# Kernel tuning notes

Measured on AMD Instinct MI355X. Metric: run time of the kernel, lower is better.

## Reference

```python
import jax, jax.numpy as jnp
from jax import lax
import numpy as np

VOCAB = 50257
EMB = 768
HID = [1024, 1024, 1024]
B, S = 2, 2048
LN_EPS_RNN = 1e-5   # torch default inside MinGRU layers
LN_EPS_OUT = 0.0    # NLPModel passes bias=False into LayerNorm's eps slot


def _layernorm(x, w, b, eps):
    mu = jnp.mean(x, axis=-1, keepdims=True)
    var = jnp.var(x, axis=-1, keepdims=True)
    return (x - mu) * lax.rsqrt(var + eps) * w + b


def _log_g(x):
    # log of g(x) = where(x>=0, x+0.5, sigmoid(x)), computed stably in log space
    return jnp.where(x >= 0, jnp.log(jax.nn.relu(x) + 0.5), -jax.nn.softplus(-x))


def _mingru_scan(gate, hidden, h0):
    # gate, hidden: [B,S,H]; h0: [B,1,H] (positive). Log-space parallel scan.
    log_coeffs = -jax.nn.softplus(gate)              # log(1-z)
    log_values = -jax.nn.softplus(-gate) + _log_g(hidden)  # log(z) + log g(h~)
    log_coeffs = jnp.pad(log_coeffs, ((0, 0), (1, 0), (0, 0)))
    log_values = jnp.concatenate([jnp.log(h0), log_values], axis=1)
    a_star = jnp.cumsum(log_coeffs, axis=1)
    log_h = a_star + lax.cumlogsumexp(log_values - a_star, axis=1)
    return jnp.exp(log_h)[:, 1:]                     # [B,S,H]


def setup_inputs() -> dict:
    key = jax.random.key(0)
    ks = jax.random.split(key, 8)
    inp = {}
    inp["ids"] = jax.random.randint(ks[0], (B, S), 0, VOCAB)
    inp["emb_W"] = jax.random.normal(ks[1], (VOCAB, EMB)) * 0.02
    dims = [EMB] + HID
    for l, (i, o) in enumerate(zip(dims[:-1], dims[1:])):
        inp[f"ln{l}_w"] = jnp.ones((i,))
        inp[f"ln{l}_b"] = jnp.zeros((i,))
        inp[f"gates{l}_W"] = jax.random.normal(jax.random.fold_in(key, 10 + l), (2 * o, i)) * (1.0 / np.sqrt(i))
    inp["res0_W"] = jax.random.normal(ks[2], (HID[0], EMB)) * (1.0 / np.sqrt(EMB))
    inp["lnf_w"] = jnp.ones((HID[-1],))
    inp["lnf_b"] = jnp.zeros((HID[-1],))
    inp["fc_W"] = jax.random.normal(ks[3], (VOCAB, HID[-1])) * 0.02
    inp["fc_b"] = jnp.zeros((VOCAB,))
    return inp


def reference(ids, emb_W, ln0_w, ln0_b, gates0_W, res0_W,
              ln1_w, ln1_b, gates1_W, ln2_w, ln2_b, gates2_W,
              lnf_w, lnf_b, fc_W, fc_b):
    x = emb_W[ids]                                   # [B,S,EMB]
    layers = [
        (ln0_w, ln0_b, gates0_W, res0_W),
        (ln1_w, ln1_b, gates1_W, None),
        (ln2_w, ln2_b, gates2_W, None),
    ]
    inp = x
    for ln_w, ln_b, gW, resW in layers:
        out_dim = gW.shape[0] // 2
        xn = _layernorm(inp, ln_w, ln_b, LN_EPS_RNN)
        gh = jnp.einsum('bsi,oi->bso', xn, gW)       # bias=False for minGRU
        gate, hidden = jnp.split(gh, 2, axis=-1)
        h0 = jnp.full((inp.shape[0], 1, out_dim), 0.5, dtype=inp.dtype)  # g(0)=0.5
        out = _mingru_scan(gate, hidden, h0)
        res = inp if resW is None else jnp.einsum('bsi,oi->bso', inp, resW)
        inp = out + res                              # residual, dropout=0
    x = _layernorm(inp, lnf_w, lnf_b, LN_EPS_OUT)
    logits = jnp.einsum('bsh,vh->bsv', x, fc_W) + fc_b
    return logits
```

## Files before the change

kernel.cpp:

```cpp
#include <hip/hip_runtime.h>
#include <stdint.h>
#include <stddef.h>


typedef __attribute__((ext_vector_type(4))) float f32x4;
typedef __attribute__((ext_vector_type(8))) short bf16x8;
typedef __attribute__((ext_vector_type(4))) unsigned short u16x4;
typedef float f32x4u __attribute__((vector_size(16), aligned(4)));

__device__ __forceinline__ unsigned short f2bf(float f) {
  unsigned int u = __float_as_uint(f);
  u += 0x7FFFu + ((u >> 16) & 1u);
  return (unsigned short)(u >> 16);
}
__device__ __forceinline__ float bf2f(unsigned short u) {
  return __uint_as_float(((unsigned int)u) << 16);
}

__device__ __forceinline__ void gload16(const void* g, void* l) {
  __builtin_amdgcn_global_load_lds(
      (const __attribute__((address_space(1))) void*)g,
      (__attribute__((address_space(3))) void*)l, 16, 0, 0);
}

#define MEMFENCE asm volatile("" ::: "memory")

__global__ __launch_bounds__(256) void cvt_kernel(
    const float* __restrict__ in, unsigned short* __restrict__ out, int n8) {
  int i = blockIdx.x * 256 + threadIdx.x;
  int stride = gridDim.x * 256;
  for (; i < n8; i += stride) {
    const float4* p = (const float4*)in + (size_t)i * 2;
    float4 a = p[0], b = p[1];
    bf16x8 o;
    o[0] = (short)f2bf(a.x); o[1] = (short)f2bf(a.y);
    o[2] = (short)f2bf(a.z); o[3] = (short)f2bf(a.w);
    o[4] = (short)f2bf(b.x); o[5] = (short)f2bf(b.y);
    o[6] = (short)f2bf(b.z); o[7] = (short)f2bf(b.w);
    *(bf16x8*)(out + (size_t)i * 8) = o;
  }
}

__global__ __launch_bounds__(256) void embed_kernel(
    const int* __restrict__ ids, const float* __restrict__ embW,
    unsigned short* __restrict__ xbf) {
  int tok = blockIdx.x;
  int id = ids[tok];
  const float* src = embW + (size_t)id * 768;
  unsigned short* dst = xbf + (size_t)tok * 768;
  for (int j = threadIdx.x; j < 768; j += 256) dst[j] = f2bf(src[j]);
}

template <int BF16IN, int D>
__global__ __launch_bounds__(256) void ln_kernel(
    const void* __restrict__ xin, const float* __restrict__ w,
    const float* __restrict__ b, unsigned short* __restrict__ xout,
    float eps) {
  constexpr int NV = D / 256;
  int row = blockIdx.x;
  int tid = threadIdx.x;
  int lane = tid & 63, wid = tid >> 6;
  const float* xf = (const float*)xin;
  const unsigned short* xb = (const unsigned short*)xin;
  float vals[NV];
  float s = 0.f, ss = 0.f;
#pragma unroll
  for (int i = 0; i < NV; i++) {
    size_t idx = (size_t)row * D + i * 256 + tid;
    float v = BF16IN ? bf2f(xb[idx]) : xf[idx];
    vals[i] = v;
    s += v;
    ss += v * v;
  }
  for (int off = 32; off; off >>= 1) {
    s += __shfl_down(s, off);
    ss += __shfl_down(ss, off);
  }
  __shared__ float red[8];
  if (lane == 0) { red[wid] = s; red[4 + wid] = ss; }
  __syncthreads();
  s = red[0] + red[1] + red[2] + red[3];
  ss = red[4] + red[5] + red[6] + red[7];
  constexpr float invD = 1.f / (float)D;
  float mu = s * invD;
  float var = ss * invD - mu * mu;
  float inv = rsqrtf(var + eps);
#pragma unroll
  for (int i = 0; i < NV; i++) {
    int col = i * 256 + tid;
    size_t idx = (size_t)row * D + col;
    float y = (vals[i] - mu) * inv * w[col] + b[col];
    xout[idx] = f2bf(y);
  }
}

template <int BF16OUT>
__global__ __launch_bounds__(256) void gemm_bt(
    const unsigned short* __restrict__ A, const unsigned short* __restrict__ B,
    void* __restrict__ Cout, int M, int N, int K) {
  __shared__ __align__(16) char smem[16896];
  unsigned short* lsA = (unsigned short*)smem;
  unsigned short* lsB = (unsigned short*)(smem + 8192);
  float* lsC = (float*)smem;

  const int tid = threadIdx.x;
  const int lane = tid & 63;
  const int wid = __builtin_amdgcn_readfirstlane(tid >> 6);
  const int row0 = blockIdx.y * 128;
  const int col0 = blockIdx.x * 128;

  const int srow = tid >> 2;
  const int skg = (tid & 3) * 8;

  const unsigned short* gA0 = A + (size_t)(row0 + srow) * K + skg;
  const unsigned short* gA1 = A + (size_t)(row0 + 64 + srow) * K + skg;
  const unsigned short* gB0 = B + (size_t)(col0 + srow) * K + skg;
  const unsigned short* gB1 = B + (size_t)(col0 + 64 + srow) * K + skg;

  char* ldsA0 = (char*)lsA + wid * 1024;
  char* ldsA1 = (char*)lsA + 4096 + wid * 1024;
  char* ldsB0 = (char*)lsB + wid * 1024;
  char* ldsB1 = (char*)lsB + 4096 + wid * 1024;

  const int wm = wid >> 1, wn = wid & 1;
  const unsigned short* pA = lsA + (wm * 64 + (lane & 15)) * 32 + (lane >> 4) * 8;
  const unsigned short* pB = lsB + (wn * 64 + (lane & 15)) * 32 + (lane >> 4) * 8;

  f32x4 acc[4][4] = {};

  for (int k0 = 0; k0 < K; k0 += 32) {
    gload16(gA0 + k0, ldsA0);
    gload16(gA1 + k0, ldsA1);
    gload16(gB0 + k0, ldsB0);
    gload16(gB1 + k0, ldsB1);
    __syncthreads();
    bf16x8 af[4], bfr[4];
#pragma unroll
    for (int i = 0; i < 4; i++) af[i] = *(const bf16x8*)(pA + i * 512);
#pragma unroll
    for (int i = 0; i < 4; i++) bfr[i] = *(const bf16x8*)(pB + i * 512);
#pragma unroll
    for (int i = 0; i < 4; i++)
#pragma unroll
      for (int j = 0; j < 4; j++)
        acc[i][j] = __builtin_amdgcn_mfma_f32_16x16x32_bf16(bfr[j], af[i],
                                                            acc[i][j], 0, 0, 0);
    __syncthreads();
  }

  const int mloc = lane & 15;
  const int ng = (lane >> 4) * 4;
  const int LDC = 132;
  const int trow = tid >> 5;
  const int tcol = (tid & 31) * 4;
#pragma unroll
  for (int c = 0; c < 4; c++) {
    if (wm == (c >> 1)) {
      const int i0 = 2 * (c & 1);
#pragma unroll
      for (int ii = 0; ii < 2; ii++)
#pragma unroll
        for (int j = 0; j < 4; j++)
          *(f32x4*)(lsC + (ii * 16 + mloc) * LDC + wn * 64 + j * 16 + ng) =
              acc[i0 + ii][j];
    }
    __syncthreads();
#pragma unroll
    for (int rr = 0; rr < 4; rr++) {
      const int r = rr * 8 + trow;
      const size_t gr = row0 + c * 32 + r;
      f32x4 v = *(const f32x4*)(lsC + r * LDC + tcol);
      if (!BF16OUT) {
        *(f32x4*)((float*)Cout + gr * N + col0 + tcol) = v;
      } else {
        u16x4 o;
#pragma unroll
        for (int q = 0; q < 4; q++) o[q] = f2bf(v[q]);
        *(u16x4*)((unsigned short*)Cout + gr * N + col0 + tcol) = o;
      }
    }
    __syncthreads();
  }
}

__global__ __launch_bounds__(512) void gemm_final256(
    const unsigned short* __restrict__ A, const unsigned short* __restrict__ B,
    float* __restrict__ C, const float* __restrict__ bias, int M, int N,
    int K) {
  __shared__ __align__(16) char smem[131072];
  float* const lsC = (float*)smem;

  const int t = threadIdx.x;
  const int l = t & 63;
  const int w = __builtin_amdgcn_readfirstlane(t >> 6);
  const int wm = w >> 2, wn = w & 3;
  const int row0 = blockIdx.x * 256;
  const int col0 = blockIdx.y * 256;

  const int srow = t >> 3;
  const int sg = ((t & 7) ^ (srow & 7)) * 8;
  const unsigned short* aS0 = A + (size_t)(row0 + srow) * K + sg;
  const unsigned short* aS1 = A + (size_t)(row0 + 64 + srow) * K + sg;
  const unsigned short* aS2 = A + (size_t)(row0 + 128 + srow) * K + sg;
  const unsigned short* aS3 = A + (size_t)(row0 + 192 + srow) * K + sg;
  int b0 = min(col0 + srow, N - 1);
  int b1 = min(col0 + 64 + srow, N - 1);
  int b2 = min(col0 + 128 + srow, N - 1);
  int b3 = min(col0 + 192 + srow, N - 1);
  const unsigned short* bS0 = B + (size_t)b0 * K + sg;
  const unsigned short* bS1 = B + (size_t)b1 * K + sg;
  const unsigned short* bS2 = B + (size_t)b2 * K + sg;
  const unsigned short* bS3 = B + (size_t)b3 * K + sg;
  const int wOff = w * 1024;

  const int aRowB = (wm * 128 + (l & 15)) * 128;
  const int bRowB = (wn * 64 + (l & 15)) * 128;
  const int gk0 = ((l >> 4) ^ (l & 7)) * 16;
  const int gk1 = ((4 + (l >> 4)) ^ (l & 7)) * 16;

  f32x4 acc[8][4] = {};

#define STAGE(BUF, KOFF)                       \
  do {                                         \
    char* a_ = smem + (BUF) * 65536;           \
    char* b_ = a_ + 32768;                     \
    gload16(aS0 + (KOFF), a_ + wOff);          \
    gload16(aS1 + (KOFF), a_ + 8192 + wOff);   \
    gload16(aS2 + (KOFF), a_ + 16384 + wOff);  \
    gload16(aS3 + (KOFF), a_ + 24576 + wOff);  \
    gload16(bS0 + (KOFF), b_ + wOff);          \
    gload16(bS1 + (KOFF), b_ + 8192 + wOff);   \
    gload16(bS2 + (KOFF), b_ + 16384 + wOff);  \
    gload16(bS3 + (KOFF), b_ + 24576 + wOff);  \
  } while (0)

  STAGE(0, 0);

  const int NK = K >> 6;
  for (int kt = 0; kt < NK; ++kt) {
    const int cur = kt & 1;
    const char* aB = smem + cur * 65536;
    const char* bB = aB + 32768;

    if (kt + 1 < NK) {
      STAGE(cur ^ 1, (kt + 1) << 6);
      asm volatile("s_waitcnt vmcnt(8)" ::: "memory");
    } else {
      asm volatile("s_waitcnt vmcnt(0)" ::: "memory");
    }
    __builtin_amdgcn_s_barrier();
    MEMFENCE;

    bf16x8 bf[4][2];
#pragma unroll
    for (int j = 0; j < 4; j++) {
      bf[j][0] = *(const bf16x8*)(bB + bRowB + j * 2048 + gk0);
      bf[j][1] = *(const bf16x8*)(bB + bRowB + j * 2048 + gk1);
    }
#pragma unroll
    for (int h = 0; h < 2; h++) {
      bf16x8 af[4][2];
#pragma unroll
      for (int i = 0; i < 4; i++) {
        af[i][0] = *(const bf16x8*)(aB + aRowB + (h * 4 + i) * 2048 + gk0);
        af[i][1] = *(const bf16x8*)(aB + aRowB + (h * 4 + i) * 2048 + gk1);
      }
#pragma unroll
      for (int i = 0; i < 4; i++)
#pragma unroll
        for (int j = 0; j < 4; j++) {
          acc[h * 4 + i][j] = __builtin_amdgcn_mfma_f32_16x16x32_bf16(
              bf[j][0], af[i][0], acc[h * 4 + i][j], 0, 0, 0);
          acc[h * 4 + i][j] = __builtin_amdgcn_mfma_f32_16x16x32_bf16(
              bf[j][1], af[i][1], acc[h * 4 + i][j], 0, 0, 0);
        }
    }

    MEMFENCE;
    __builtin_amdgcn_s_barrier();
    MEMFENCE;
  }
#undef STAGE

  const int mloc = l & 15;
  const int ng = (l >> 4) * 4;
  const int LDC = 260;
#pragma unroll
  for (int c = 0; c < 8; c++) {
    if (wm == (c >> 2)) {
      const int fr0 = (c & 3) * 2;
#pragma unroll
      for (int ii = 0; ii < 2; ii++)
#pragma unroll
        for (int j = 0; j < 4; j++)
          *(f32x4*)(lsC + (ii * 16 + mloc) * LDC + wn * 64 + j * 16 + ng) =
              acc[fr0 + ii][j];
    }
    __syncthreads();
#pragma unroll
    for (int rr = 0; rr < 4; rr++) {
      const int r = rr * 8 + (t >> 6);
      const size_t gr = row0 + c * 32 + r;
      f32x4 v = *(const f32x4*)(lsC + r * LDC + (t & 63) * 4);
      const int n0 = col0 + (t & 63) * 4;
      if (col0 + 256 <= N) {
        const f32x4u bv = *(const f32x4u*)(bias + n0);
        f32x4u o;
#pragma unroll
        for (int q = 0; q < 4; q++) o[q] = v[q] + bv[q];
        __builtin_nontemporal_store(o, (f32x4u*)(C + gr * N + n0));
      } else {
#pragma unroll
        for (int q = 0; q < 4; q++)
          if (n0 + q < N) C[gr * N + n0 + q] = v[q] + bias[n0 + q];
      }
    }
    __syncthreads();
  }
}

__device__ __forceinline__ void gru_step(float gate, float hid, float& a,
                                         float& g) {
  a = 1.f / (1.f + expf(gate));
  g = (hid >= 0.f) ? (hid + 0.5f) : 1.f / (1.f + expf(-hid));
}

__global__ __launch_bounds__(256) void scan_compose(
    const unsigned short* __restrict__ gh, float* __restrict__ Acl,
    float* __restrict__ Vcl) {
  int ck = blockIdx.x;
  int hp = blockIdx.y * 256 + threadIdx.x;
  int b = hp >> 10, h = hp & 1023;
  const unsigned short* gb = gh + ((size_t)(b * 2048 + ck * 64)) * 2048 + h;
  float A = 1.f, V = 0.f;
  for (int t = 0; t < 64; t++) {
    float gate = bf2f(gb[(size_t)t * 2048]);
    float hid = bf2f(gb[(size_t)t * 2048 + 1024]);
    float a, g;
    gru_step(gate, hid, a, g);
    V = a * V + (1.f - a) * g;
    A *= a;
  }
  size_t i = (size_t)(b * 32 + ck) * 1024 + h;
  Acl[i] = A;
  Vcl[i] = V;
}

__global__ __launch_bounds__(256) void scan_prefix(
    const float* __restrict__ Acl, const float* __restrict__ Vcl,
    float* __restrict__ Hin) {
  int hp = blockIdx.x * 256 + threadIdx.x;
  int b = hp >> 10, h = hp & 1023;
  float hr = 0.5f;
  for (int ck = 0; ck < 32; ck++) {
    size_t i = (size_t)(b * 32 + ck) * 1024 + h;
    Hin[i] = hr;
    hr = Acl[i] * hr + Vcl[i];
  }
}

template <int RESBF>
__global__ __launch_bounds__(256) void scan_emit(
    const unsigned short* __restrict__ gh, const float* __restrict__ Hin,
    const void* __restrict__ res, float* __restrict__ xout) {
  int ck = blockIdx.x;
  int hp = blockIdx.y * 256 + threadIdx.x;
  int b = hp >> 10, h = hp & 1023;
  const unsigned short* gb = gh + ((size_t)(b * 2048 + ck * 64)) * 2048 + h;
  const size_t rbase = ((size_t)(b * 2048 + ck * 64)) * 1024 + h;
  const unsigned short* rb16 = (const unsigned short*)res + rbase;
  const float* rb32 = (const float*)res + rbase;
  float* ob = xout + rbase;
  float hc = Hin[(size_t)(b * 32 + ck) * 1024 + h];
  for (int t = 0; t < 64; t++) {
    float gate = bf2f(gb[(size_t)t * 2048]);
    float hid = bf2f(gb[(size_t)t * 2048 + 1024]);
    float a, g;
    gru_step(gate, hid, a, g);
    hc = a * hc + (1.f - a) * g;
    float r = RESBF ? bf2f(rb16[(size_t)t * 1024]) : rb32[(size_t)t * 1024];
    ob[(size_t)t * 1024] = hc + r;
  }
}

extern "C" void kernel_launch(void* const* d_in, const int* in_sizes, int n_in,
                              void* d_out, int out_size, void* d_ws,
                              size_t ws_size, hipStream_t stream) {
  (void)in_sizes; (void)n_in; (void)out_size; (void)ws_size;
  const int* ids = (const int*)d_in[0];
  const float* embW = (const float*)d_in[1];
  const float* ln0w = (const float*)d_in[2];
  const float* ln0b = (const float*)d_in[3];
  const float* g0W = (const float*)d_in[4];
  const float* ln1w = (const float*)d_in[5];
  const float* ln1b = (const float*)d_in[6];
  const float* g1W = (const float*)d_in[7];
  const float* ln2w = (const float*)d_in[8];
  const float* ln2b = (const float*)d_in[9];
  const float* g2W = (const float*)d_in[10];
  const float* r0W = (const float*)d_in[11];
  const float* lnfw = (const float*)d_in[12];
  const float* lnfb = (const float*)d_in[13];
  const float* fcW = (const float*)d_in[14];
  const float* fcb = (const float*)d_in[15];
  float* out = (float*)d_out;

  const int M = 4096;
  const int V = 50257;

  char* ws = (char*)d_ws;
  unsigned short* x_bf = (unsigned short*)(ws + 0);
  float* x_f = (float*)(ws + 6291456);
  unsigned short* xn_bf = (unsigned short*)(ws + 23068672);
  unsigned short* gh_bf = (unsigned short*)(ws + 31457280);
  unsigned short* r0_bf = (unsigned short*)(ws + 48234496);
  float* Acl = (float*)(ws + 56623104);
  float* Vcl = (float*)(ws + 56885248);
  float* Hin = (float*)(ws + 57147392);
  unsigned short* gwbf = (unsigned short*)(ws + 57409536);
  unsigned short* rwbf = (unsigned short*)(ws + 61603840);
  unsigned short* fcwbf = (unsigned short*)(ws + 63176704);

  auto cvt = [&](const float* src, unsigned short* dst, int n) {
    int n8 = n / 8;
    int grid = min((n8 + 255) / 256, 2048);
    cvt_kernel<<<grid, 256, 0, stream>>>(src, dst, n8);
  };

  embed_kernel<<<M, 256, 0, stream>>>(ids, embW, x_bf);
  cvt(fcW, fcwbf, V * 1024);
  cvt(r0W, rwbf, 1024 * 768);

  cvt(g0W, gwbf, 2048 * 768);
  ln_kernel<1, 768><<<M, 256, 0, stream>>>(x_bf, ln0w, ln0b, xn_bf, 1e-5f);
  gemm_bt<1><<<dim3(16, 32), 256, 0, stream>>>(xn_bf, gwbf, gh_bf, M, 2048,
                                               768);
  gemm_bt<1><<<dim3(8, 32), 256, 0, stream>>>(x_bf, rwbf, r0_bf, M, 1024, 768);
  scan_compose<<<dim3(32, 8), 256, 0, stream>>>(gh_bf, Acl, Vcl);
  scan_prefix<<<8, 256, 0, stream>>>(Acl, Vcl, Hin);
  scan_emit<1><<<dim3(32, 8), 256, 0, stream>>>(gh_bf, Hin, r0_bf, x_f);

  cvt(g1W, gwbf, 2048 * 1024);
  ln_kernel<0, 1024><<<M, 256, 0, stream>>>(x_f, ln1w, ln1b, xn_bf, 1e-5f);
  gemm_bt<1><<<dim3(16, 32), 256, 0, stream>>>(xn_bf, gwbf, gh_bf, M, 2048,
                                               1024);
  scan_compose<<<dim3(32, 8), 256, 0, stream>>>(gh_bf, Acl, Vcl);
  scan_prefix<<<8, 256, 0, stream>>>(Acl, Vcl, Hin);
  scan_emit<0><<<dim3(32, 8), 256, 0, stream>>>(gh_bf, Hin, x_f, x_f);

  cvt(g2W, gwbf, 2048 * 1024);
  ln_kernel<0, 1024><<<M, 256, 0, stream>>>(x_f, ln2w, ln2b, xn_bf, 1e-5f);
  gemm_bt<1><<<dim3(16, 32), 256, 0, stream>>>(xn_bf, gwbf, gh_bf, M, 2048,
                                               1024);
  scan_compose<<<dim3(32, 8), 256, 0, stream>>>(gh_bf, Acl, Vcl);
  scan_prefix<<<8, 256, 0, stream>>>(Acl, Vcl, Hin);
  scan_emit<0><<<dim3(32, 8), 256, 0, stream>>>(gh_bf, Hin, x_f, x_f);

  ln_kernel<0, 1024><<<M, 256, 0, stream>>>(x_f, lnfw, lnfb, xn_bf, 0.0f);
  gemm_final256<<<dim3(16, (V + 255) / 256), 512, 0, stream>>>(
      xn_bf, fcwbf, out, fcb, M, V, 1024);
}
```

Before: 889.0 us.

## Fuse fc_W fp32-to-bf16 conversion into final logits GEMM B-tile loading

Drops the standalone conversion pass over the large vocabulary projection weight. The final GEMM now reads fp32 weights directly into registers, packs them to bf16 with v_cvt_pk_bf16_f32 and stores them into swizzled LDS. This removes a full write and re-read of the converted weight. In exchange, each tile re-reads fp32 data (double bytes) across all row blocks, and the async LDS-direct load for B is replaced by a register-staged prefetch with a full vmcnt wait.

```diff
diff --git a/kernel.cpp b/kernel.cpp
--- a/kernel.cpp
+++ b/kernel.cpp
@@ -6,6 +6,7 @@
 typedef __attribute__((ext_vector_type(4))) float f32x4;
 typedef __attribute__((ext_vector_type(8))) short bf16x8;
 typedef __attribute__((ext_vector_type(4))) unsigned short u16x4;
+typedef __attribute__((ext_vector_type(4))) unsigned int u32x4;
 typedef float f32x4u __attribute__((vector_size(16), aligned(4)));
 
 __device__ __forceinline__ unsigned short f2bf(float f) {
@@ -15,6 +16,11 @@
 }
 __device__ __forceinline__ float bf2f(unsigned short u) {
   return __uint_as_float(((unsigned int)u) << 16);
+}
+__device__ __forceinline__ unsigned int cvt_pk_bf16(float lo, float hi) {
+  unsigned int r;
+  asm("v_cvt_pk_bf16_f32 %0, %1, %2" : "=v"(r) : "v"(lo), "v"(hi));
+  return r;
 }
 
 __device__ __forceinline__ void gload16(const void* g, void* l) {
@@ -184,7 +190,7 @@
 }
 
 __global__ __launch_bounds__(512) void gemm_final256(
-    const unsigned short* __restrict__ A, const unsigned short* __restrict__ B,
+    const unsigned short* __restrict__ A, const float* __restrict__ Bf,
     float* __restrict__ C, const float* __restrict__ bias, int M, int N,
     int K) {
   __shared__ __align__(16) char smem[131072];
@@ -203,14 +209,17 @@
   const unsigned short* aS1 = A + (size_t)(row0 + 64 + srow) * K + sg;
   const unsigned short* aS2 = A + (size_t)(row0 + 128 + srow) * K + sg;
   const unsigned short* aS3 = A + (size_t)(row0 + 192 + srow) * K + sg;
-  int b0 = min(col0 + srow, N - 1);
-  int b1 = min(col0 + 64 + srow, N - 1);
-  int b2 = min(col0 + 128 + srow, N - 1);
-  int b3 = min(col0 + 192 + srow, N - 1);
-  const unsigned short* bS0 = B + (size_t)b0 * K + sg;
-  const unsigned short* bS1 = B + (size_t)b1 * K + sg;
-  const unsigned short* bS2 = B + (size_t)b2 * K + sg;
-  const unsigned short* bS3 = B + (size_t)b3 * K + sg;
+
+  const int sgB = (t & 7) * 8;
+  int r0i = min(col0 + srow, N - 1);
+  int r1i = min(col0 + 64 + srow, N - 1);
+  int r2i = min(col0 + 128 + srow, N - 1);
+  int r3i = min(col0 + 192 + srow, N - 1);
+  const float* bF0 = Bf + (size_t)r0i * K + sgB;
+  const float* bF1 = Bf + (size_t)r1i * K + sgB;
+  const float* bF2 = Bf + (size_t)r2i * K + sgB;
+  const float* bF3 = Bf + (size_t)r3i * K + sgB;
+  const int bWr = srow * 128 + (((t & 7) ^ (srow & 7)) * 16);
   const int wOff = w * 1024;
 
   const int aRowB = (wm * 128 + (l & 15)) * 128;
@@ -219,37 +228,62 @@
   const int gk1 = ((4 + (l >> 4)) ^ (l & 7)) * 16;
 
   f32x4 acc[8][4] = {};
-
-#define STAGE(BUF, KOFF)                       \
+  float4 br[8];
+
+#define STAGE_A(BUF, KOFF)                     \
   do {                                         \
     char* a_ = smem + (BUF) * 65536;           \
-    char* b_ = a_ + 32768;                     \
     gload16(aS0 + (KOFF), a_ + wOff);          \
     gload16(aS1 + (KOFF), a_ + 8192 + wOff);   \
     gload16(aS2 + (KOFF), a_ + 16384 + wOff);  \
     gload16(aS3 + (KOFF), a_ + 24576 + wOff);  \
-    gload16(bS0 + (KOFF), b_ + wOff);          \
-    gload16(bS1 + (KOFF), b_ + 8192 + wOff);   \
-    gload16(bS2 + (KOFF), b_ + 16384 + wOff);  \
-    gload16(bS3 + (KOFF), b_ + 24576 + wOff);  \
   } while (0)
 
-  STAGE(0, 0);
+#define BLOAD(KOFF)                                  \
+  do {                                               \
+    br[0] = *(const float4*)(bF0 + (KOFF));          \
+    br[1] = *(const float4*)(bF0 + (KOFF) + 4);      \
+    br[2] = *(const float4*)(bF1 + (KOFF));          \
+    br[3] = *(const float4*)(bF1 + (KOFF) + 4);      \
+    br[4] = *(const float4*)(bF2 + (KOFF));          \
+    br[5] = *(const float4*)(bF2 + (KOFF) + 4);      \
+    br[6] = *(const float4*)(bF3 + (KOFF));          \
+    br[7] = *(const float4*)(bF3 + (KOFF) + 4);      \
+  } while (0)
+
+#define BWRITE(BUF)                                            \
+  do {                                                         \
+    char* b_ = smem + (BUF) * 65536 + 32768;                   \
+    _Pragma("unroll") for (int i_ = 0; i_ < 4; ++i_) {         \
+      u32x4 o_;                                                \
+      o_[0] = cvt_pk_bf16(br[2 * i_].x, br[2 * i_].y);         \
+      o_[1] = cvt_pk_bf16(br[2 * i_].z, br[2 * i_].w);         \
+      o_[2] = cvt_pk_bf16(br[2 * i_ + 1].x, br[2 * i_ + 1].y); \
+      o_[3] = cvt_pk_bf16(br[2 * i_ + 1].z, br[2 * i_ + 1].w); \
+      *(u32x4*)(b_ + i_ * 8192 + bWr) = o_;                    \
+    }                                                          \
+  } while (0)
+
+  BLOAD(0);
+  STAGE_A(0, 0);
+  asm volatile("s_waitcnt vmcnt(0)" ::: "memory");
+  BWRITE(0);
+  asm volatile("s_waitcnt lgkmcnt(0)" ::: "memory");
+  __builtin_amdgcn_s_barrier();
+  MEMFENCE;
 
   const int NK = K >> 6;
   for (int kt = 0; kt < NK; ++kt) {
     const int cur = kt & 1;
     const char* aB = smem + cur * 65536;
     const char* bB = aB + 32768;
-
-    if (kt + 1 < NK) {
-      STAGE(cur ^ 1, (kt + 1) << 6);
-      asm volatile("s_waitcnt vmcnt(8)" ::: "memory");
-    } else {
-      asm volatile("s_waitcnt vmcnt(0)" ::: "memory");
-    }
-    __builtin_amdgcn_s_barrier();
-    MEMFENCE;
+    const bool pre = (kt + 1 < NK);
+    const int kN = (kt + 1) << 6;
+
+    if (pre) {
+      BLOAD(kN);
+      STAGE_A(cur ^ 1, kN);
+    }
 
     bf16x8 bf[4][2];
 #pragma unroll
@@ -276,11 +310,17 @@
         }
     }
 
-    MEMFENCE;
+    if (pre) {
+      asm volatile("s_waitcnt vmcnt(0)" ::: "memory");
+      BWRITE(cur ^ 1);
+    }
+    asm volatile("s_waitcnt lgkmcnt(0)" ::: "memory");
     __builtin_amdgcn_s_barrier();
     MEMFENCE;
   }
-#undef STAGE
+#undef STAGE_A
+#undef BLOAD
+#undef BWRITE
 
   const int mloc = l & 15;
   const int ng = (l >> 4) * 4;
@@ -419,7 +459,6 @@
   float* Hin = (float*)(ws + 57147392);
   unsigned short* gwbf = (unsigned short*)(ws + 57409536);
   unsigned short* rwbf = (unsigned short*)(ws + 61603840);
-  unsigned short* fcwbf = (unsigned short*)(ws + 63176704);
 
   auto cvt = [&](const float* src, unsigned short* dst, int n) {
     int n8 = n / 8;
@@ -428,7 +467,6 @@
   };
 
   embed_kernel<<<M, 256, 0, stream>>>(ids, embW, x_bf);
-  cvt(fcW, fcwbf, V * 1024);
   cvt(r0W, rwbf, 1024 * 768);
 
   cvt(g0W, gwbf, 2048 * 768);
@@ -458,5 +496,5 @@
 
   ln_kernel<0, 1024><<<M, 256, 0, stream>>>(x_f, lnfw, lnfb, xn_bf, 0.0f);
   gemm_final256<<<dim3(16, (V + 255) / 256), 512, 0, stream>>>(
-      xn_bf, fcwbf, out, fcb, M, V, 1024);
-}
+      xn_bf, fcW, out, fcb, M, V, 1024);
+}
```

Result: slower. 981.4 us (+10.4%).
